# Optimization experiments

Measured on AMD Instinct MI355X. Metric: run time of the kernel, lower is better.

The kernel has to match this reference:

```python
import jax, jax.numpy as jnp
import numpy as np

N = 100000      # total nodes across all graphs
E = 1600000     # total directed edges (pred -> node)
F = 128         # feat_size
H = 128         # hidden_size
M = 128         # message_size
G = 8           # number of graphs in batch
NP = N // G     # nodes per graph (num_nodes entries, all equal)
CRITIC_W = 0.5  # critic_agg_weight


def _lin_init(key, fan_in, fan_out):
    s = 1.0 / np.sqrt(fan_in)
    return jax.random.uniform(key, (fan_in, fan_out), jnp.float32, -s, s)


def setup_inputs() -> dict:
    key = jax.random.key(0)
    ks = jax.random.split(key, 20)
    inputs = jax.random.normal(ks[0], (N, F), jnp.float32)
    edge_src = jax.random.randint(ks[1], (E,), 0, N)
    edge_dst = jax.random.randint(ks[2], (E,), 0, N)
    actions = jax.random.randint(ks[3], (G,), 0, NP)
    return {
        'inputs': inputs,
        'W_in': _lin_init(ks[4], F, H), 'b_in': jnp.zeros((H,), jnp.float32),
        'W_msg': _lin_init(ks[5], H, M), 'b_msg': jnp.zeros((M,), jnp.float32),
        'W_upd': _lin_init(ks[6], M + H, H), 'b_upd': jnp.zeros((H,), jnp.float32),
        'W_a1': _lin_init(ks[7], H, 16), 'b_a1': jnp.zeros((16,), jnp.float32),
        'W_a2': _lin_init(ks[8], 16, 1), 'b_a2': jnp.zeros((1,), jnp.float32),
        'W_c1': _lin_init(ks[9], H, 16), 'b_c1': jnp.zeros((16,), jnp.float32),
        'W_c2': _lin_init(ks[10], 16, 1), 'b_c2': jnp.zeros((1,), jnp.float32),
        'edge_src': edge_src, 'edge_dst': edge_dst, 'actions': actions,
    }


def reference(inputs, W_in, b_in, W_msg, b_msg, W_upd, b_upd,
              W_a1, b_a1, W_a2, b_a2, W_c1, b_c1, W_c2, b_c2,
              edge_src, edge_dst, actions):
    # InputModel: Linear + ReLU  (send_input=True)
    node_states = jax.nn.relu(inputs @ W_in + b_in)          # [N, H]
    # MessageModel: Linear + ReLU
    messages = jax.nn.relu(node_states @ W_msg + b_msg)      # [N, M]
    # _aggregate_all: per-node sum over predecessor messages (segment-sum over edges)
    agg = jax.ops.segment_sum(messages[edge_src], edge_dst, num_segments=N)  # [N, M]
    # UpdateModel: Linear(M+H, H) + ReLU (no goal)
    updates = jax.nn.relu(jnp.concatenate([agg, node_states], axis=1) @ W_upd + b_upd)  # [N, H]
    # ActorModel: per-node logit
    logits_all = (jax.nn.relu(updates @ W_a1 + b_a1) @ W_a2 + b_a2).reshape(G, NP)
    # CriticModel: per-node score, per-graph weighted max/mean pooling
    crit_all = (jax.nn.relu(updates @ W_c1 + b_c1) @ W_c2 + b_c2).reshape(G, NP)
    v = (crit_all.max(axis=1) * CRITIC_W + crit_all.mean(axis=1) * (1.0 - CRITIC_W))[:, None]  # [G,1]
    # Categorical(logits) per graph: log_prob of given action + entropy
    logp = jax.nn.log_softmax(logits_all, axis=1)            # [G, NP]
    log_prob = jnp.take_along_axis(logp, actions[:, None], axis=1)  # [G,1]
    ent = -jnp.sum(jnp.exp(logp) * logp, axis=1, keepdims=True)     # [G,1]
    return updates, actions, log_prob, ent, v
```

## Files before the change

### kernel.cpp

```cpp
#include <hip/hip_runtime.h>
#include <math.h>

typedef unsigned short u16;
typedef unsigned int   u32;
typedef unsigned char  u8;
typedef __attribute__((ext_vector_type(8))) short short8v;
typedef __attribute__((ext_vector_type(4))) float f32x4;
typedef __attribute__((ext_vector_type(2))) float f32x2;

__device__ __forceinline__ u16 f2bf(float x) {
    u32 u = __float_as_uint(x);
    u += 0x7FFFu + ((u >> 16) & 1u);
    return (u16)(u >> 16);
}

#if __has_builtin(__builtin_amdgcn_cvt_pk_fp8_f32) && __has_builtin(__builtin_amdgcn_cvt_pk_f32_fp8)
#define HW_FP8 1
#endif

__device__ __forceinline__ u8 f2fp8(float v) {
#ifdef HW_FP8
    return (u8)(__builtin_amdgcn_cvt_pk_fp8_f32(v, v, 0, false) & 0xFF);
#else
    if (v < 0.015625f) return (u8)__float2int_rn(v * 512.0f);
    u32 b = __float_as_uint(fminf(v, 448.0f));
    b += 0x7FFFF + ((b >> 20) & 1);
    return (u8)((((b >> 23) - 120) << 3) | ((b >> 20) & 7));
#endif
}

__device__ __forceinline__ void fp8x4_acc(u32 w, float* acc) {
#ifdef HW_FP8
    const f32x2 lo = __builtin_amdgcn_cvt_pk_f32_fp8(w, false);
    const f32x2 hi = __builtin_amdgcn_cvt_pk_f32_fp8(w, true);
    acc[0] += lo[0]; acc[1] += lo[1]; acc[2] += hi[0]; acc[3] += hi[1];
#else
#pragma unroll
    for (int i = 0; i < 4; ++i) {
        const u32 b = (w >> (8 * i)) & 0xFF;
        const u32 e = (b >> 3) & 15, m = b & 7;
        acc[i] += e ? __uint_as_float(((e + 120) << 23) | (m << 20))
                    : (float)m * 0x1p-9f;
    }
#endif
}

#define NPB        256
#define NPB_SHIFT  8
#define EBUF_CAP   4608
#define MAX_BUK    512
#define BCS        16

__global__ __launch_bounds__(256) void convbin_kernel(
    const float* __restrict__ W_in, const float* __restrict__ W_msg,
    const float* __restrict__ W_upd,
    const float* __restrict__ Wa1, const float* __restrict__ Wc1,
    u16* __restrict__ Wt_in, u16* __restrict__ Wt_msg,
    u16* __restrict__ Wt_upd, u16* __restrict__ Wh,
    const int* __restrict__ src, const int* __restrict__ dst,
    int* __restrict__ bcursor, int* __restrict__ ebuf,
    int E, int nbuk, int chunk, int convBlocks)
{
    __shared__ int lcount[MAX_BUK];
    __shared__ int lbase[MAX_BUK];
    const int tid = threadIdx.x;

    if ((int)blockIdx.x < convBlocks) {
        const int idx = blockIdx.x * 256 + tid;
        if (idx < 16384) {
            const int c = idx >> 7, k = idx & 127;
            Wt_in[c * 128 + k] = f2bf(W_in[k * 128 + c]);
        } else if (idx < 32768) {
            const int i = idx - 16384;
            const int c = i >> 7, k = i & 127;
            Wt_msg[c * 128 + k] = f2bf(W_msg[k * 128 + c]);
        } else if (idx < 65536) {
            const int i = idx - 32768;
            const int c = i >> 8, k = i & 255;
            Wt_upd[c * 256 + k] = f2bf(W_upd[k * 128 + c]);
        } else if (idx < 69632) {
            const int i = idx - 65536;
            const int col = i >> 7, k = i & 127;
            const float v = (col < 16) ? Wa1[k * 16 + col] : Wc1[k * 16 + (col - 16)];
            Wh[col * 128 + k] = f2bf(v);
        }
        return;
    }

    const int e0 = (blockIdx.x - convBlocks) * chunk;
    const int e1 = min(e0 + chunk, E);
    for (int b = tid; b < nbuk; b += 256) lcount[b] = 0;
    __syncthreads();
    for (int i = e0 + tid; i < e1; i += 256)
        atomicAdd(&lcount[dst[i] >> NPB_SHIFT], 1);
    __syncthreads();
    for (int b = tid; b < nbuk; b += 256) {
        const int c = lcount[b];
        lbase[b] = c ? atomicAdd(&bcursor[b * BCS], c) : 0;
        lcount[b] = 0;
    }
    __syncthreads();
    for (int i = e0 + tid; i < e1; i += 256) {
        const int d = dst[i];
        const int b = d >> NPB_SHIFT;
        const int p = lbase[b] + atomicAdd(&lcount[b], 1);
        ebuf[b * EBUF_CAP + min(p, EBUF_CAP - 1)] = (src[i] << NPB_SHIFT) | (d & (NPB - 1));
    }
}

__global__ __launch_bounds__(256) void csr_gemm1_kernel(
    const int* __restrict__ ebuf, const int* __restrict__ bcursor,
    int* __restrict__ offs, int* __restrict__ csr, int N, int E, int nbuk,
    const float* __restrict__ X, const u16* __restrict__ Wt_in,
    const float* __restrict__ b_in, u16* __restrict__ ns, int rows)
{
    __shared__ u16 smem[128 * 136];
    const int tid = threadIdx.x;

    if ((int)blockIdx.x < nbuk) {
        int* ibuf = (int*)smem;
        int* red  = ibuf;
        int* ndeg = ibuf + 4;
        int* nofs = ibuf + 260;
        int* ws   = ibuf + 516;
        int* wp   = ibuf + 520;
        const int b = blockIdx.x;

        int part = 0;
        for (int i = tid; i < b; i += 256) part += bcursor[i * BCS];
#pragma unroll
        for (int off = 32; off >= 1; off >>= 1) part += __shfl_xor(part, off);
        if ((tid & 63) == 0) red[tid >> 6] = part;
        __syncthreads();
        const int base = red[0] + red[1] + red[2] + red[3];

        const int cnt = min(bcursor[b * BCS], EBUF_CAP);
        const int* eb = ebuf + b * EBUF_CAP;

        ndeg[tid] = 0;
        __syncthreads();
        for (int j = tid; j < cnt; j += 256)
            atomicAdd(&ndeg[eb[j] & (NPB - 1)], 1);
        __syncthreads();

        const int lane = tid & 63, wid = tid >> 6;
        const int v = ndeg[tid];
        int x = v;
#pragma unroll
        for (int off = 1; off < 64; off <<= 1) {
            const int y = __shfl_up(x, off);
            if (lane >= off) x += y;
        }
        if (lane == 63) ws[wid] = x;
        __syncthreads();
        if (tid == 0) { int s = 0; for (int w = 0; w < 4; ++w) { wp[w] = s; s += ws[w]; } }
        __syncthreads();
        const int excl = x - v + wp[wid];
        nofs[tid] = excl;
        const int node = (b << NPB_SHIFT) + tid;
        if (node < N) offs[node] = base + excl;
        if (b == 0 && tid == 0) offs[N] = E;
        ndeg[tid] = 0;
        __syncthreads();

        for (int j = tid; j < cnt; j += 256) {
            const int e = eb[j];
            const int d = e & (NPB - 1);
            const int p = atomicAdd(&ndeg[d], 1);
            csr[base + nofs[d] + p] = e >> NPB_SHIFT;
        }
        return;
    }

    u16 (*WtL)[136] = (u16(*)[136])smem;
    for (int i = tid; i < 2048; i += 256)
        *(uint4*)&WtL[i >> 4][(i & 15) * 8] = ((const uint4*)Wt_in)[i];

    const int lane = tid & 63, wave = tid >> 6;
    const int lrow = lane & 15, lk = lane >> 4;
    const int r0 = (blockIdx.x - nbuk) * 64 + wave * 16;
    const int arow = r0 + lrow;
    const bool rowok = arow < rows;

    short8v a[4];
#pragma unroll
    for (int ks = 0; ks < 4; ++ks) {
        const int k = ks * 32 + lk * 8;
        short8v av = {};
        if (rowok) {
            const float* pf = X + (size_t)arow * 128 + k;
            const float4 x0 = *(const float4*)pf;
            const float4 x1 = *(const float4*)(pf + 4);
            u16 t[8] = {f2bf(x0.x), f2bf(x0.y), f2bf(x0.z), f2bf(x0.w),
                        f2bf(x1.x), f2bf(x1.y), f2bf(x1.z), f2bf(x1.w)};
            av = *(short8v*)t;
        }
        a[ks] = av;
    }
    __syncthreads();

    f32x4 acc[8];
#pragma unroll
    for (int n = 0; n < 8; ++n) acc[n] = (f32x4){0.f, 0.f, 0.f, 0.f};
#pragma unroll
    for (int ks = 0; ks < 4; ++ks) {
#pragma unroll
        for (int n = 0; n < 8; ++n) {
            const short8v b = *(const short8v*)&WtL[n * 16 + lrow][ks * 32 + lk * 8];
            acc[n] = __builtin_amdgcn_mfma_f32_16x16x32_bf16(a[ks], b, acc[n], 0, 0, 0);
        }
    }
#pragma unroll
    for (int reg = 0; reg < 4; ++reg) {
        const int row = r0 + lk * 4 + reg;
        if (row >= rows) continue;
#pragma unroll
        for (int n = 0; n < 8; ++n) {
            const float v = fmaxf(acc[n][reg] + b_in[n * 16 + lrow], 0.f);
            ns[(size_t)row * 128 + n * 16 + lrow] = f2bf(v);
        }
    }
}

__global__ __launch_bounds__(512) void gemm2_kernel(
    const u16* __restrict__ ns, const u16* __restrict__ Wt_msg,
    const float* __restrict__ b_msg, u8* __restrict__ msg8, int rows)
{
    __shared__ u16 smem[128 * 136];
    u16 (*WtL)[136] = (u16(*)[136])smem;
    const int tid = threadIdx.x;
    for (int i = tid; i < 2048; i += 512)
        *(uint4*)&WtL[i >> 4][(i & 15) * 8] = ((const uint4*)Wt_msg)[i];

    const int lane = tid & 63, wave = tid >> 6;
    const int lrow = lane & 15, lk = lane >> 4;
    const int r0 = blockIdx.x * 128 + wave * 16;
    const int arow = r0 + lrow;
    const bool rowok = arow < rows;

    short8v a[4];
#pragma unroll
    for (int ks = 0; ks < 4; ++ks) {
        short8v av = {};
        if (rowok) av = *(const short8v*)(ns + (size_t)arow * 128 + ks * 32 + lk * 8);
        a[ks] = av;
    }
    __syncthreads();

    f32x4 acc[8];
#pragma unroll
    for (int n = 0; n < 8; ++n) acc[n] = (f32x4){0.f, 0.f, 0.f, 0.f};
#pragma unroll
    for (int ks = 0; ks < 4; ++ks) {
#pragma unroll
        for (int n = 0; n < 8; ++n) {
            const short8v b = *(const short8v*)&WtL[n * 16 + lrow][ks * 32 + lk * 8];
            acc[n] = __builtin_amdgcn_mfma_f32_16x16x32_bf16(a[ks], b, acc[n], 0, 0, 0);
        }
    }
#pragma unroll
    for (int reg = 0; reg < 4; ++reg) {
        const int row = r0 + lk * 4 + reg;
        if (row >= rows) continue;
#pragma unroll
        for (int n = 0; n < 8; ++n) {
            const float v = fmaxf(acc[n][reg] + b_msg[n * 16 + lrow], 0.f);
            msg8[(size_t)row * 128 + n * 16 + lrow] = f2fp8(v);
        }
    }
}

__device__ __forceinline__ void acc16(float* acc, const uint4 u) {
    fp8x4_acc(u.x, acc);
    fp8x4_acc(u.y, acc + 4);
    fp8x4_acc(u.z, acc + 8);
    fp8x4_acc(u.w, acc + 12);
}

__global__ __launch_bounds__(256) void gather_fp8_kernel(
    const int* __restrict__ offs, const int* __restrict__ csr,
    const u8* __restrict__ msg8, u16* __restrict__ agg, int N)
{
    const int node = blockIdx.x * 32 + (threadIdx.x >> 3);
    if (node >= N) return;
    const int c16 = threadIdx.x & 7;
    int j = offs[node];
    const int j1 = offs[node + 1];
    const uint4* mv = (const uint4*)msg8;
    float acc[16];
#pragma unroll
    for (int q = 0; q < 16; ++q) acc[q] = 0.f;
    for (; j + 3 < j1; j += 4) {
        const int s0 = csr[j], s1 = csr[j + 1], s2 = csr[j + 2], s3 = csr[j + 3];
        const uint4 u0 = mv[(size_t)s0 * 8 + c16];
        const uint4 u1 = mv[(size_t)s1 * 8 + c16];
        const uint4 u2 = mv[(size_t)s2 * 8 + c16];
        const uint4 u3 = mv[(size_t)s3 * 8 + c16];
        acc16(acc, u0); acc16(acc, u1); acc16(acc, u2); acc16(acc, u3);
    }
    for (; j < j1; ++j)
        acc16(acc, mv[(size_t)csr[j] * 8 + c16]);

    u16 r[16];
#pragma unroll
    for (int q = 0; q < 16; ++q) r[q] = f2bf(acc[q]);
    uint4* ap = (uint4*)(agg + (size_t)node * 128 + c16 * 16);
    ap[0] = *(uint4*)r;
    ap[1] = *(uint4*)(r + 8);
}

__global__ __launch_bounds__(512) void gemm3_head_kernel(
    const u16* __restrict__ agg, const u16* __restrict__ ns,
    const u16* __restrict__ Wt_upd, const float* __restrict__ b_upd,
    float* __restrict__ Cf,
    const u16* __restrict__ Wh,
    const float* __restrict__ ba1, const float* __restrict__ Wa2, const float* __restrict__ ba2,
    const float* __restrict__ bc1, const float* __restrict__ Wc2, const float* __restrict__ bc2,
    float* __restrict__ logits, float* __restrict__ crit, int rows)
{
    __shared__ u16 smem[128 * 136];
    u16 (*WtL)[136] = (u16(*)[136])smem;

    const int tid = threadIdx.x;
    const uint4* W4 = (const uint4*)Wt_upd;

    for (int i = tid; i < 2048; i += 512)
        *(uint4*)&WtL[i >> 4][(i & 15) * 8] = W4[(i >> 4) * 32 + (i & 15)];

    const int lane = tid & 63, wave = tid >> 6;
    const int lrow = lane & 15, lk = lane >> 4;
    const int r0 = blockIdx.x * 128 + wave * 16;
    const int arow = r0 + lrow;
    const bool rowok = arow < rows;

    short8v a[4], a2[4];
#pragma unroll
    for (int ks = 0; ks < 4; ++ks) {
        short8v av = {}, av2 = {};
        if (rowok) {
            av  = *(const short8v*)(agg + (size_t)arow * 128 + ks * 32 + lk * 8);
            av2 = *(const short8v*)(ns  + (size_t)arow * 128 + ks * 32 + lk * 8);
        }
        a[ks] = av; a2[ks] = av2;
    }
    __syncthreads();

    f32x4 acc[8];
#pragma unroll
    for (int n = 0; n < 8; ++n) acc[n] = (f32x4){0.f, 0.f, 0.f, 0.f};
#pragma unroll
    for (int ks = 0; ks < 4; ++ks) {
#pragma unroll
        for (int n = 0; n < 8; ++n) {
            const short8v b = *(const short8v*)&WtL[n * 16 + lrow][ks * 32 + lk * 8];
            acc[n] = __builtin_amdgcn_mfma_f32_16x16x32_bf16(a[ks], b, acc[n], 0, 0, 0);
        }
    }

    __syncthreads();
    for (int i = tid; i < 2048; i += 512)
        *(uint4*)&WtL[i >> 4][(i & 15) * 8] = W4[(i >> 4) * 32 + 16 + (i & 15)];
    __syncthreads();

#pragma unroll
    for (int ks = 0; ks < 4; ++ks) {
#pragma unroll
        for (int n = 0; n < 8; ++n) {
            const short8v b = *(const short8v*)&WtL[n * 16 + lrow][ks * 32 + lk * 8];
            acc[n] = __builtin_amdgcn_mfma_f32_16x16x32_bf16(a2[ks], b, acc[n], 0, 0, 0);
        }
    }

    u16 uv[4][8];
#pragma unroll
    for (int reg = 0; reg < 4; ++reg) {
        const int row = r0 + lk * 4 + reg;
#pragma unroll
        for (int n = 0; n < 8; ++n) {
            const float v = fmaxf(acc[n][reg] + b_upd[n * 16 + lrow], 0.f);
            uv[reg][n] = f2bf(v);
            if (row < rows) Cf[(size_t)row * 128 + n * 16 + lrow] = v;
        }
    }
    __syncthreads();

    u16 (*uT)[16][136] = (u16(*)[16][136])smem;
#pragma unroll
    for (int reg = 0; reg < 4; ++reg) {
        const int lr = lk * 4 + reg;
#pragma unroll
        for (int n = 0; n < 8; ++n)
            uT[wave][lr][n * 16 + lrow] = uv[reg][n];
    }
    __syncthreads();

    short8v ah[4], b0[4], b1[4];
#pragma unroll
    for (int ks = 0; ks < 4; ++ks) {
        const int k = ks * 32 + lk * 8;
        ah[ks] = *(const short8v*)&uT[wave][lrow][k];
        b0[ks] = *(const short8v*)(Wh + (size_t)lrow * 128 + k);
        b1[ks] = *(const short8v*)(Wh + (size_t)(16 + lrow) * 128 + k);
    }
    f32x4 acc0 = (f32x4){0.f, 0.f, 0.f, 0.f};
    f32x4 acc1 = (f32x4){0.f, 0.f, 0.f, 0.f};
#pragma unroll
    for (int ks = 0; ks < 4; ++ks) {
        acc0 = __builtin_amdgcn_mfma_f32_16x16x32_bf16(ah[ks], b0[ks], acc0, 0, 0, 0);
        acc1 = __builtin_amdgcn_mfma_f32_16x16x32_bf16(ah[ks], b1[ks], acc1, 0, 0, 0);
    }
    const float wa = Wa2[lrow], wc = Wc2[lrow];
    const float ha = ba1[lrow], hc = bc1[lrow];
    const float b2a = ba2[0],   b2c = bc2[0];
#pragma unroll
    for (int reg = 0; reg < 4; ++reg) {
        float pa = fmaxf(acc0[reg] + ha, 0.f) * wa;
        float pc = fmaxf(acc1[reg] + hc, 0.f) * wc;
#pragma unroll
        for (int off = 8; off >= 1; off >>= 1) {
            pa += __shfl_xor(pa, off);
            pc += __shfl_xor(pc, off);
        }
        const int row = r0 + lk * 4 + reg;
        if (lrow == 0 && row < rows) {
            logits[row] = pa + b2a;
            crit[row]   = pc + b2c;
        }
    }
}

__device__ __forceinline__ float blockRedMax(float v, float* red) {
#pragma unroll
    for (int o = 32; o >= 1; o >>= 1) v = fmaxf(v, __shfl_xor(v, o));
    const int w = threadIdx.x >> 6;
    __syncthreads();
    if ((threadIdx.x & 63) == 0) red[w] = v;
    __syncthreads();
    if (threadIdx.x < 16) {
        float x = red[threadIdx.x];
#pragma unroll
        for (int o = 8; o >= 1; o >>= 1) x = fmaxf(x, __shfl_xor(x, o));
        if (threadIdx.x == 0) red[0] = x;
    }
    __syncthreads();
    const float r = red[0];
    __syncthreads();
    return r;
}

__device__ __forceinline__ float blockRedSum(float v, float* red) {
#pragma unroll
    for (int o = 32; o >= 1; o >>= 1) v += __shfl_xor(v, o);
    const int w = threadIdx.x >> 6;
    __syncthreads();
    if ((threadIdx.x & 63) == 0) red[w] = v;
    __syncthreads();
    if (threadIdx.x < 16) {
        float x = red[threadIdx.x];
#pragma unroll
        for (int o = 8; o >= 1; o >>= 1) x += __shfl_xor(x, o);
        if (threadIdx.x == 0) red[0] = x;
    }
    __syncthreads();
    const float r = red[0];
    __syncthreads();
    return r;
}

__global__ __launch_bounds__(1024) void finalize_kernel(
    const float* __restrict__ logits, const float* __restrict__ crit,
    const int* __restrict__ actions, float* __restrict__ out, int NP, int G)
{
    __shared__ float slog[12512];
    __shared__ float red[16];
    const int g = blockIdx.x;
    const int tid = threadIdx.x;
    const float* lg = logits + (long long)g * NP;
    const float* cg = crit   + (long long)g * NP;

    float lmax = -3.402823466e38f, cmax = -3.402823466e38f, csum = 0.f;
    for (int i = tid; i < NP; i += 1024) {
        const float l = lg[i], c = cg[i];
        slog[i] = l;
        lmax = fmaxf(lmax, l);
        cmax = fmaxf(cmax, c);
        csum += c;
    }
    __syncthreads();
    lmax = blockRedMax(lmax, red);
    cmax = blockRedMax(cmax, red);
    csum = blockRedSum(csum, red);

    float zsum = 0.f, ssum = 0.f;
    for (int i = tid; i < NP; i += 1024) {
        const float s = slog[i];
        const float e = expf(s - lmax);
        zsum += e;
        ssum += s * e;
    }
    zsum = blockRedSum(zsum, red);
    ssum = blockRedSum(ssum, red);

    if (tid == 0) {
        const int a = actions[g];
        const float sa   = slog[a];
        const float logZ = logf(zsum) + lmax;
        const float lp   = sa - logZ;
        const float H    = logZ - ssum / zsum;
        const float v    = cmax * 0.5f + (csum / (float)NP) * 0.5f;
        out[g]         = (float)a;
        out[G + g]     = lp;
        out[2 * G + g] = H;
        out[3 * G + g] = v;
    }
}

extern "C" void kernel_launch(void* const* d_in, const int* in_sizes, int n_in,
                              void* d_out, int out_size, void* d_ws, size_t ws_size,
                              hipStream_t stream)
{
    const float* inputs = (const float*)d_in[0];
    const float* W_in   = (const float*)d_in[1];
    const float* b_in   = (const float*)d_in[2];
    const float* W_msg  = (const float*)d_in[3];
    const float* b_msg  = (const float*)d_in[4];
    const float* W_upd  = (const float*)d_in[5];
    const float* b_upd  = (const float*)d_in[6];
    const float* W_a1   = (const float*)d_in[7];
    const float* b_a1   = (const float*)d_in[8];
    const float* W_a2   = (const float*)d_in[9];
    const float* b_a2   = (const float*)d_in[10];
    const float* W_c1   = (const float*)d_in[11];
    const float* b_c1   = (const float*)d_in[12];
    const float* W_c2   = (const float*)d_in[13];
    const float* b_c2   = (const float*)d_in[14];
    const int* edge_src = (const int*)d_in[15];
    const int* edge_dst = (const int*)d_in[16];
    const int* actions  = (const int*)d_in[17];

    const int N  = in_sizes[0] / 128;
    const int E  = in_sizes[15];
    const int G  = in_sizes[17];
    const int NP = N / G;
    const int nbuk = (N + NPB - 1) >> NPB_SHIFT;

    float* out = (float*)d_out;

    u16* ns_bf  = (u16*)d_ws;
    u16* agg_bf = ns_bf + (size_t)N * 128;
    u8*  msg8   = (u8*)(agg_bf + (size_t)N * 128);
    u16* Wt_in  = (u16*)(msg8 + (size_t)N * 128);
    u16* Wt_msg = Wt_in  + 128 * 128;
    u16* Wt_upd = Wt_msg + 128 * 128;
    u16* Wh     = Wt_upd + 128 * 256;
    float* logits = (float*)(Wh + 32 * 128);
    float* crit   = logits + N;
    int*   offs    = (int*)(crit + N);
    int*   csr     = offs + (N + 1);
    int*   bcursor = csr + E;
    int*   ebuf    = bcursor + MAX_BUK * BCS;

    const int chunk = 8192;
    const int binGrid    = (E + chunk - 1) / chunk;
    const int convBlocks = 69632 / 256;
    const int gemmGrid   = (N + 63) / 64;
    const int gemmGrid2  = (N + 127) / 128;

    hipMemsetAsync(bcursor, 0, (size_t)MAX_BUK * BCS * sizeof(int), stream);
    convbin_kernel<<<convBlocks + binGrid, 256, 0, stream>>>(
        W_in, W_msg, W_upd, W_a1, W_c1, Wt_in, Wt_msg, Wt_upd, Wh,
        edge_src, edge_dst, bcursor, ebuf, E, nbuk, chunk, convBlocks);
    csr_gemm1_kernel<<<nbuk + gemmGrid, 256, 0, stream>>>(
        ebuf, bcursor, offs, csr, N, E, nbuk,
        inputs, Wt_in, b_in, ns_bf, N);
    gemm2_kernel<<<gemmGrid2, 512, 0, stream>>>(ns_bf, Wt_msg, b_msg, msg8, N);
    gather_fp8_kernel<<<(N + 31) / 32, 256, 0, stream>>>(offs, csr, msg8, agg_bf, N);
    gemm3_head_kernel<<<gemmGrid2, 512, 0, stream>>>(
        agg_bf, ns_bf, Wt_upd, b_upd, out, Wh,
        b_a1, W_a2, b_a2, b_c1, W_c2, b_c2, logits, crit, N);
    finalize_kernel<<<G, 1024, 0, stream>>>(logits, crit, actions, out + (size_t)N * 128, NP, G);
}
```

Before: 168.3 us.

## Bin edges in registers with one-pass local rank and smaller chunks

The edge-binning phase now gives each block 1024 edges, four per thread, kept in registers. The local atomic that counts a bucket also returns the edge's rank within it, so the second pass over dst/src and the second round of shared atomics are gone. Blocks grow from about 196 to about 1563, which spreads the binning across more CUs. In exchange there are many more global atomics on bcursor (one per nonempty bucket per block) and lower write locality into ebuf.

```diff
diff --git a/kernel.cpp b/kernel.cpp
--- a/kernel.cpp
+++ b/kernel.cpp
@@ -50,6 +50,7 @@
 #define EBUF_CAP   4608
 #define MAX_BUK    512
 #define BCS        16
+#define BIN_CHUNK  1024
 
 __global__ __launch_bounds__(256) void convbin_kernel(
     const float* __restrict__ W_in, const float* __restrict__ W_msg,
@@ -59,7 +60,7 @@
     u16* __restrict__ Wt_upd, u16* __restrict__ Wh,
     const int* __restrict__ src, const int* __restrict__ dst,
     int* __restrict__ bcursor, int* __restrict__ ebuf,
-    int E, int nbuk, int chunk, int convBlocks)
+    int E, int nbuk, int convBlocks)
 {
     __shared__ int lcount[MAX_BUK];
     __shared__ int lbase[MAX_BUK];
@@ -87,24 +88,41 @@
         return;
     }
 
-    const int e0 = (blockIdx.x - convBlocks) * chunk;
-    const int e1 = min(e0 + chunk, E);
+    const int e0 = (blockIdx.x - convBlocks) * BIN_CHUNK;
+    const int e1 = min(e0 + BIN_CHUNK, E);
     for (int b = tid; b < nbuk; b += 256) lcount[b] = 0;
     __syncthreads();
-    for (int i = e0 + tid; i < e1; i += 256)
-        atomicAdd(&lcount[dst[i] >> NPB_SHIFT], 1);
-    __syncthreads();
+
+    int pay[4];
+    u32 brk[4];
+#pragma unroll
+    for (int k = 0; k < 4; ++k) {
+        const int i = e0 + tid + k * 256;
+        int payv = 0; u32 brkv = 0xFFFFFFFFu;
+        if (i < e1) {
+            const int d = dst[i];
+            const int b = d >> NPB_SHIFT;
+            const int r = atomicAdd(&lcount[b], 1);
+            payv = (src[i] << NPB_SHIFT) | (d & (NPB - 1));
+            brkv = ((u32)b << 16) | (u32)r;
+        }
+        pay[k] = payv; brk[k] = brkv;
+    }
+    __syncthreads();
+
     for (int b = tid; b < nbuk; b += 256) {
         const int c = lcount[b];
         lbase[b] = c ? atomicAdd(&bcursor[b * BCS], c) : 0;
-        lcount[b] = 0;
-    }
-    __syncthreads();
-    for (int i = e0 + tid; i < e1; i += 256) {
-        const int d = dst[i];
-        const int b = d >> NPB_SHIFT;
-        const int p = lbase[b] + atomicAdd(&lcount[b], 1);
-        ebuf[b * EBUF_CAP + min(p, EBUF_CAP - 1)] = (src[i] << NPB_SHIFT) | (d & (NPB - 1));
+    }
+    __syncthreads();
+
+#pragma unroll
+    for (int k = 0; k < 4; ++k) {
+        if (brk[k] != 0xFFFFFFFFu) {
+            const int b = (int)(brk[k] >> 16);
+            const int p = lbase[b] + (int)(brk[k] & 0xFFFFu);
+            ebuf[b * EBUF_CAP + min(p, EBUF_CAP - 1)] = pay[k];
+        }
     }
 }
 
@@ -560,8 +578,7 @@
     int*   bcursor = csr + E;
     int*   ebuf    = bcursor + MAX_BUK * BCS;
 
-    const int chunk = 8192;
-    const int binGrid    = (E + chunk - 1) / chunk;
+    const int binGrid    = (E + BIN_CHUNK - 1) / BIN_CHUNK;
     const int convBlocks = 69632 / 256;
     const int gemmGrid   = (N + 63) / 64;
     const int gemmGrid2  = (N + 127) / 128;
@@ -569,7 +586,7 @@
     hipMemsetAsync(bcursor, 0, (size_t)MAX_BUK * BCS * sizeof(int), stream);
     convbin_kernel<<<convBlocks + binGrid, 256, 0, stream>>>(
         W_in, W_msg, W_upd, W_a1, W_c1, Wt_in, Wt_msg, Wt_upd, Wh,
-        edge_src, edge_dst, bcursor, ebuf, E, nbuk, chunk, convBlocks);
+        edge_src, edge_dst, bcursor, ebuf, E, nbuk, convBlocks);
     csr_gemm1_kernel<<<nbuk + gemmGrid, 256, 0, stream>>>(
         ebuf, bcursor, offs, csr, N, E, nbuk,
         inputs, Wt_in, b_in, ns_bf, N);
```

Result: slower. 192.1 us (+14.1%).
